# Kernel optimization log

Hardware: AMD Instinct MI355X
Metric: run time of the kernel (lower is better)

Reference implementation:

```python
import jax, jax.numpy as jnp
import numpy as np

K = 3            # CRF kernel size
THETA0 = 0.5     # color bandwidth
THETA1 = 30.0    # spatial bandwidth
ALPHA0 = 3.0     # kernel scale
BASE = 0.45      # label clamping base
CRF_ITERS = 10   # mean-field iterations
NMS_SIGMA = 2.0  # gaussian matrix-NMS sigma


def _unfold(x, k=K):
    # torch.nn.Unfold(k, stride=1, padding=k//2): (B, C, H, W) -> (B, C, k*k, H*W)
    B, C, H, W = x.shape
    p = k // 2
    xp = jnp.pad(x, ((0, 0), (0, 0), (p, p), (p, p)))
    patches = jnp.stack([xp[:, :, i:i + H, j:j + W]
                         for i in range(k) for j in range(k)], axis=2)
    return patches.reshape(B, C, k * k, H * W)


def _matrix_nms(seg_masks, cate_labels, cate_scores, sigma=NMS_SIGMA):
    n = seg_masks.shape[0]
    m = seg_masks.reshape(n, -1).astype(jnp.float32)
    sum_m = m.sum(axis=1)                         # (n,)
    inter = m @ m.T                               # (n, n)
    union = sum_m[None, :] + sum_m[:, None] - inter
    triu = jnp.triu(jnp.ones((n, n), dtype=bool), k=1)
    iou = jnp.where(triu, inter / union, 0.0)
    label_eq = (cate_labels[None, :] == cate_labels[:, None]) & triu
    decay_iou = jnp.where(label_eq, iou, 0.0)
    comp = decay_iou.max(axis=0)                  # compensate IoU per candidate
    decay = jnp.exp(-sigma * decay_iou ** 2)
    compm = jnp.exp(-sigma * comp ** 2)[:, None]  # broadcast over columns (torch expand+T)
    coef = (decay / compm).min(axis=0)
    return cate_scores * coef


def _crf(feature_map, x, targets):
    B, C, H, W = feature_map.shape
    k2 = K * K
    # gaussian pairwise kernel from (shifted) color features
    fm = feature_map + 10.0
    uf = _unfold(fm)                              # (B, C, k2, H*W)
    idx = np.arange(k2)
    spatial = ((idx // K - K // 2) ** 2 + (idx % K - K // 2) ** 2).astype(np.float32)
    color = -((uf - fm.reshape(B, C, 1, H * W)) ** 2).sum(axis=1) / (2.0 * THETA0 ** 2)
    kernel = ALPHA0 * jnp.exp(color - jnp.asarray(spatial)[None, :, None] / (2.0 * THETA1 ** 2))
    kernel = kernel[:, None]                      # (B, 1, k2, H*W)

    # unary init
    xt = x * targets
    xt = (xt > 0.5).astype(jnp.float32) * (1.0 - 2.0 * BASE) + BASE
    ret = jnp.concatenate([1.0 - xt, xt], axis=1)  # (B, 2, H, W)
    ones_t = jnp.ones_like(targets)
    for _ in range(CRF_ITERS):
        uf_x = _unfold(-jnp.log(ret.reshape(2 * B, 1, H, W))).reshape(B, 2, k2, H * W)
        aggre = (uf_x * kernel).sum(axis=2)        # (B, 2, H*W)
        f = jnp.exp(-aggre).reshape(B, 2, H, W)
        f = f * jnp.concatenate([ones_t, targets], axis=1)  # gate fg channel by targets
        f = f + 1e-6
        f = f / f.sum(axis=1, keepdims=True)
        ret = (f > 0.5).astype(jnp.float32) * (1.0 - 2.0 * BASE) + BASE
    masks = (ret[:, 1:] > 0.5).astype(jnp.float32)  # (B, 1, H, W)
    count = masks.reshape(B, -1).sum(axis=1)
    valid = ((count >= H * W * 0.05) & (count <= H * W * 0.95)).astype(jnp.float32)
    return masks, valid


def setup_inputs() -> dict:
    key = jax.random.key(0)
    k1, k2, k3, k4, k5, k6 = jax.random.split(key, 6)
    n, h, w = 256, 128, 128
    ni, c = 64, 3
    seg_masks = (jax.random.uniform(k1, (n, h, w)) > 0.5).astype(jnp.float32)
    cate_scores = jnp.sort(jax.random.uniform(k2, (n,)))[::-1]
    feature_map = jax.random.uniform(k3, (ni, c, h, w))
    x = jax.random.uniform(k4, (ni, 1, h, w))
    targets = (jax.random.uniform(k5, (ni, 1, h, w)) > 0.3).astype(jnp.float32)
    cate_labels = jax.random.randint(k6, (n,), 0, 80, dtype=jnp.int64)
    return {"seg_masks": seg_masks, "cate_scores": cate_scores,
            "feature_map": feature_map, "x": x, "targets": targets,
            "cate_labels": cate_labels}


def reference(seg_masks, cate_scores, feature_map, x, targets, cate_labels):
    scores = _matrix_nms(seg_masks, cate_labels, cate_scores)
    masks, valid = _crf(feature_map, x, targets)
    return scores, masks, valid
```

## Files before the change

kernel.cpp:

```cpp
#include <hip/hip_runtime.h>
#include <stdint.h>

#define HW 16384
#define NI 64
#define NM 256
#define WORDS 256

#define PR 136
#define WROWS 52
#define PSZ (WROWS * PR)
#define SR 34

#define LDS_PLANE_BYTES (4 * PSZ * 4)
#define LDS_STW_BYTES   (2 * WROWS * SR * 4)
#define LDS_TOTAL       (LDS_PLANE_BYTES + LDS_STW_BYTES + 64)

#define OFF_PACKED (2u << 20)
#define OFF_DIOUT  0x280000u
#define OFF_COMPM  0x2C0000u
#define OFF_CNT    0x2C1000u

__device__ __forceinline__ void build_planes_row(
    const float* __restrict__ fb, float* __restrict__ plane, const int y,
    const int xc, const int wrow, const int q, const bool inimg) {
    #pragma clang fp contract(off)
    float c0[4], c1[4], c2[4];
    if (inimg) {
        const int pp = y * 128 + xc;
        float4 cv0 = *(const float4*)&fb[pp];
        float4 cv1 = *(const float4*)&fb[HW + pp];
        float4 cv2 = *(const float4*)&fb[2 * HW + pp];
        c0[0]=cv0.x+10.0f; c0[1]=cv0.y+10.0f; c0[2]=cv0.z+10.0f; c0[3]=cv0.w+10.0f;
        c1[0]=cv1.x+10.0f; c1[1]=cv1.y+10.0f; c1[2]=cv1.z+10.0f; c1[3]=cv1.w+10.0f;
        c2[0]=cv2.x+10.0f; c2[1]=cv2.y+10.0f; c2[2]=cv2.z+10.0f; c2[3]=cv2.w+10.0f;
    }
    #pragma unroll
    for (int k = 0; k < 4; ++k) {
        const int dy = (k < 3) ? -1 : 0;
        const int dx = (k < 3) ? (k - 1) : -1;
        float res[4] = {0.0f, 0.0f, 0.0f, 0.0f};
        if (inimg) {
            const int ny = y + dy;
            if ((unsigned)ny < 128u) {
                #pragma unroll
                for (int j = 0; j < 4; ++j) {
                    const int nx = xc + j + dx;
                    if ((unsigned)nx < 128u) {
                        const int qq = ny * 128 + nx;
                        float u0 = fb[qq] + 10.0f;
                        float u1 = fb[HW + qq] + 10.0f;
                        float u2 = fb[2 * HW + qq] + 10.0f;
                        float d0 = u0 - c0[j], d1 = u1 - c1[j], d2 = u2 - c2[j];
                        float ss = d0 * d0;
                        ss = ss + d1 * d1;
                        ss = ss + d2 * d2;
                        float color = (-ss) / 0.5f;
                        float sp = (float)(dy * dy + dx * dx) / 1800.0f;
                        res[j] = 3.0f * expf(color - sp);
                    }
                }
            }
        }
        *(float4*)&plane[k * PSZ + wrow * PR + 4 + xc] =
            make_float4(res[0], res[1], res[2], res[3]);
        if (q == 0)
            *(float4*)&plane[k * PSZ + wrow * PR + 0] = make_float4(0, 0, 0, 0);
        if (q == 31)
            *(float4*)&plane[k * PSZ + wrow * PR + 132] = make_float4(0, 0, 0, 0);
    }
}

__device__ __forceinline__ void stage_init_row(
    const float* __restrict__ x, const float* __restrict__ targets,
    uint32_t* __restrict__ stw0, uint32_t* __restrict__ stw1, const int img,
    const int y, const int wrow, const int q, const int xc, const bool inimg) {
    #pragma clang fp contract(off)
    uint32_t st = 0;
    if (inimg) {
        const size_t gp = (size_t)img * HW + y * 128 + xc;
        const float4 xv = *(const float4*)(x + gp);
        const float4 tv = *(const float4*)(targets + gp);
        float xs[4] = {xv.x, xv.y, xv.z, xv.w};
        float ts[4] = {tv.x, tv.y, tv.z, tv.w};
        #pragma unroll
        for (int j = 0; j < 4; ++j) {
            float xt = xs[j] * ts[j];
            int b1 = (xt > 0.5f) ? 1 : 0;
            int tb = (ts[j] > 0.5f) ? 1 : 0;
            st |= (uint32_t)(b1 | ((b1 ^ 1) << 1) | (tb << 2)) << (8 * j);
        }
    }
    stw0[wrow * SR + 1 + q] = st;
    if (!inimg) stw1[wrow * SR + 1 + q] = 0;
    if (q == 0)  { stw0[wrow * SR + 0]  = 0; stw1[wrow * SR + 0]  = 0; }
    if (q == 31) { stw0[wrow * SR + 33] = 0; stw1[wrow * SR + 33] = 0; }
}

__device__ __forceinline__ uint32_t crf_core(const float (&kw)[9][4],
                                             const uint32_t (&in9)[9]) {
    #pragma clang fp contract(off)
    const float l45 = 0.7985076962177716f;
    const float l55 = 0.5978370007556204f;
    const uint32_t wcen = in9[4];
    float lx1r[3][6], lx0r[3][6];
    #pragma unroll
    for (int r = 0; r < 3; ++r) {
        const uint32_t wm = in9[r * 3 + 0];
        const uint32_t wc = in9[r * 3 + 1];
        const uint32_t wp = in9[r * 3 + 2];
        unsigned char b[6];
        b[0] = wm >> 24;
        b[1] = wc & 0xff; b[2] = (wc >> 8) & 0xff;
        b[3] = (wc >> 16) & 0xff; b[4] = wc >> 24;
        b[5] = wp & 0xff;
        #pragma unroll
        for (int m = 0; m < 6; ++m) {
            lx1r[r][m] = (b[m] & 1) ? l55 : l45;
            lx0r[r][m] = (b[m] & 2) ? l55 : l45;
        }
    }
    float a0[4] = {0.f, 0.f, 0.f, 0.f}, a1[4] = {0.f, 0.f, 0.f, 0.f};
    #pragma unroll
    for (int k = 0; k < 9; ++k) {
        const int r = k / 3, m0 = k % 3;
        #pragma unroll
        for (int j = 0; j < 4; ++j) {
            const float kwv = kw[k][j];
            const float t1 = lx1r[r][j + m0] * kwv;
            const float t0 = lx0r[r][j + m0] * kwv;
            a1[j] = a1[j] + t1;
            a0[j] = a0[j] + t0;
        }
    }
    uint32_t ow = 0;
    #pragma unroll
    for (int j = 0; j < 4; ++j) {
        const unsigned char sc = (wcen >> (8 * j)) & 0xffu;
        const float tval = (sc & 4) ? 1.0f : 0.0f;
        const float e1 = expf(-a1[j]);
        const float e0 = expf(-a0[j]);
        const float m1 = e1 * tval;
        const float f1 = m1 + 1e-6f;
        const float f0 = e0 + 1e-6f;
        const float den = f0 + f1;
        const float r1 = f1 / den;
        const float r0v = f0 / den;
        const int s1 = (r1 > 0.5f) ? 1 : 0;
        const int s0 = (r0v > 0.5f) ? 1 : 0;
        ow |= (uint32_t)(s1 | (s0 << 1) | (sc & 4)) << (8 * j);
    }
    return ow;
}

__global__ __launch_bounds__(832, 4) void crf10_kernel(
    const float* __restrict__ feat, const float* __restrict__ seg,
    unsigned long long* __restrict__ packed, const float* __restrict__ x,
    const float* __restrict__ targets, float* __restrict__ out,
    int* __restrict__ counters) {
    #pragma clang fp contract(off)
    extern __shared__ char smem[];
    float* plane = (float*)smem;
    uint32_t* stw0 = (uint32_t*)(smem + LDS_PLANE_BYTES);
    uint32_t* stw1 = stw0 + WROWS * SR;
    int* chg = (int*)(smem + LDS_PLANE_BYTES + LDS_STW_BYTES);
    uint32_t* const stwb[2] = {stw0, stw1};

    const int tid = threadIdx.x, bid = blockIdx.x;
    const int img = bid >> 2;
    const int r0 = (bid & 3) * 32;
    const int relp = tid >> 5;
    const int q = tid & 31;
    const int xc = q * 4;
    const int wrowA = 2 * relp, wrowB = 2 * relp + 1;
    const int yA = r0 - 10 + wrowA, yB = yA + 1;
    const bool inA = (unsigned)yA < 128u, inB = (unsigned)yB < 128u;
    const int rbaseA = wrowA * PR + 4 + xc, rbaseB = wrowB * PR + 4 + xc;
    const int sbaseA = wrowA * SR + 1 + q,  sbaseB = wrowB * SR + 1 + q;
    const float* fb = feat + (size_t)img * 3 * HW;

    {
        const int wave = tid >> 6, lane = tid & 63;
        const int gw = bid * 13 + wave;
        for (int gwi = gw; gwi < 65536; gwi += 3328) {
            const int i = gwi >> 8, w = gwi & 255;
            float v = seg[(size_t)i * HW + w * 64 + lane];
            unsigned long long m = __ballot(v > 0.5f);
            if (lane == 0) packed[w * NM + i] = m;
        }
    }

    build_planes_row(fb, plane, yA, xc, wrowA, q, inA);
    build_planes_row(fb, plane, yB, xc, wrowB, q, inB);
    stage_init_row(x, targets, stw0, stw1, img, yA, wrowA, q, xc, inA);
    stage_init_row(x, targets, stw0, stw1, img, yB, wrowB, q, xc, inB);
    if (tid < 10) chg[tid] = 0;
    __syncthreads();

    const float4 a_p0 = *(const float4*)&plane[0 * PSZ + rbaseA];
    const float4 a_p1 = *(const float4*)&plane[1 * PSZ + rbaseA];
    const float4 a_p2 = *(const float4*)&plane[2 * PSZ + rbaseA];
    const float4 a_p3 = *(const float4*)&plane[3 * PSZ + rbaseA];
    const float  a_s5 = plane[3 * PSZ + rbaseA + 4];
    const float4 b_p0 = *(const float4*)&plane[0 * PSZ + rbaseB];
    const float4 b_p1 = *(const float4*)&plane[1 * PSZ + rbaseB];
    const float4 b_p2 = *(const float4*)&plane[2 * PSZ + rbaseB];
    const float4 b_p3 = *(const float4*)&plane[3 * PSZ + rbaseB];
    const float  b_s5 = plane[3 * PSZ + rbaseB + 4];
    const float  b_s6 = plane[2 * PSZ + rbaseB - 1];
    const float  b_s8 = plane[0 * PSZ + rbaseB + 4];
    const float kwA[9][4] = {
        {a_p0.x, a_p0.y, a_p0.z, a_p0.w},
        {a_p1.x, a_p1.y, a_p1.z, a_p1.w},
        {a_p2.x, a_p2.y, a_p2.z, a_p2.w},
        {a_p3.x, a_p3.y, a_p3.z, a_p3.w},
        {3.0f, 3.0f, 3.0f, 3.0f},
        {a_p3.y, a_p3.z, a_p3.w, a_s5},
        {b_s6, b_p2.x, b_p2.y, b_p2.z},
        {b_p1.x, b_p1.y, b_p1.z, b_p1.w},
        {b_p0.y, b_p0.z, b_p0.w, b_s8}};

    uint32_t pinA[9], pinB[9];
    uint32_t powvA = 0, powvB = 0;
    bool hpA = false, hpB = false;
    int cur = 0;
    for (int s = 0; s < 10; ++s) {
        const int lo = (r0 - 9 + s < 0) ? 0 : r0 - 9 + s;
        const int hi = (r0 + 41 - s > 128) ? 128 : r0 + 41 - s;
        const bool actA = (yA >= lo) && (yA < hi);
        const bool actB = (yB >= lo) && (yB < hi);
        const uint32_t* sw = stwb[cur];
        uint32_t* swn = stwb[cur ^ 1];
        bool changed = false;
        if (actA || actB) {
            const uint32_t ra0 = sw[sbaseA - 1], ra1 = sw[sbaseA], ra2 = sw[sbaseA + 1];
            const uint32_t rb0 = sw[sbaseB - 1], rb1 = sw[sbaseB], rb2 = sw[sbaseB + 1];
            if (actA) {
                const uint32_t in9[9] = {sw[sbaseA - SR - 1], sw[sbaseA - SR],
                                         sw[sbaseA - SR + 1], ra0, ra1, ra2,
                                         rb0, rb1, rb2};
                bool same = hpA;
                #pragma unroll
                for (int m = 0; m < 9; ++m) same = same && (in9[m] == pinA[m]);
                uint32_t ow;
                if (same) {
                    ow = powvA;
                } else {
                    ow = crf_core(kwA, in9);
                    #pragma unroll
                    for (int m = 0; m < 9; ++m) pinA[m] = in9[m];
                    powvA = ow;
                    hpA = true;
                }
                swn[sbaseA] = ow;
                changed = (ow != ra1);
            }
            if (actB) {
                const uint32_t in9[9] = {ra0, ra1, ra2, rb0, rb1, rb2,
                                         sw[sbaseB + SR - 1], sw[sbaseB + SR],
                                         sw[sbaseB + SR + 1]};
                bool same = hpB;
                #pragma unroll
                for (int m = 0; m < 9; ++m) same = same && (in9[m] == pinB[m]);
                uint32_t ow;
                if (same) {
                    ow = powvB;
                } else {
                    const float4 c_p0 = *(const float4*)&plane[0 * PSZ + rbaseB + PR];
                    const float4 c_p1 = *(const float4*)&plane[1 * PSZ + rbaseB + PR];
                    const float4 c_p2 = *(const float4*)&plane[2 * PSZ + rbaseB + PR];
                    const float  c_s6 = plane[2 * PSZ + rbaseB + PR - 1];
                    const float  c_s8 = plane[0 * PSZ + rbaseB + PR + 4];
                    const float kwB[9][4] = {
                        {b_p0.x, b_p0.y, b_p0.z, b_p0.w},
                        {b_p1.x, b_p1.y, b_p1.z, b_p1.w},
                        {b_p2.x, b_p2.y, b_p2.z, b_p2.w},
                        {b_p3.x, b_p3.y, b_p3.z, b_p3.w},
                        {3.0f, 3.0f, 3.0f, 3.0f},
                        {b_p3.y, b_p3.z, b_p3.w, b_s5},
                        {c_s6, c_p2.x, c_p2.y, c_p2.z},
                        {c_p1.x, c_p1.y, c_p1.z, c_p1.w},
                        {c_p0.y, c_p0.z, c_p0.w, c_s8}};
                    ow = crf_core(kwB, in9);
                    #pragma unroll
                    for (int m = 0; m < 9; ++m) pinB[m] = in9[m];
                    powvB = ow;
                    hpB = true;
                }
                swn[sbaseB] = ow;
                changed = changed || (ow != rb1);
            }
        }
        unsigned long long bal = __ballot(changed);
        if ((tid & 63) == 0 && bal) atomicOr(&chg[s], 1);
        __syncthreads();
        if (chg[s] == 0) break;
        cur ^= 1;
    }

    int cnt = 0;
    {
        const uint32_t* swf = stwb[cur];
        float* om = out + NM + (size_t)img * HW;
        if (yA >= r0 && yA < r0 + 32) {
            const uint32_t w = swf[sbaseA];
            *(float4*)(om + yA * 128 + xc) =
                make_float4((float)(w & 1), (float)((w >> 8) & 1),
                            (float)((w >> 16) & 1), (float)((w >> 24) & 1));
            cnt += __popc(w & 0x01010101u);
        }
        if (yB >= r0 && yB < r0 + 32) {
            const uint32_t w = swf[sbaseB];
            *(float4*)(om + yB * 128 + xc) =
                make_float4((float)(w & 1), (float)((w >> 8) & 1),
                            (float)((w >> 16) & 1), (float)((w >> 24) & 1));
            cnt += __popc(w & 0x01010101u);
        }
    }
    __syncthreads();
    {
        int* cred = (int*)plane;
        cred[tid] = cnt;
        if (tid < 192) cred[832 + tid] = 0;
        __syncthreads();
        for (int off = 512; off > 0; off >>= 1) {
            if (tid < off) cred[tid] += cred[tid + off];
            __syncthreads();
        }
        if (tid == 0) counters[bid] = cred[0];
    }
}

__global__ __launch_bounds__(256) void diou_compm_kernel(
    const unsigned long long* __restrict__ packed, const int* __restrict__ labels,
    float* __restrict__ diouT, float* __restrict__ compm) {
    #pragma clang fp contract(off)
    __shared__ unsigned long long colj[WORDS];
    __shared__ float red[NM];
    const int j = blockIdx.x, i = threadIdx.x;
    colj[i] = packed[i * NM + j];
    __syncthreads();
    int inter = 0, si = 0, sj = 0;
    for (int w = 0; w < WORDS; ++w) {
        unsigned long long a = colj[w];
        unsigned long long b = packed[w * NM + i];
        inter += __popcll(a & b);
        sj += __popcll(a);
        si += __popcll(b);
    }
    float d = 0.0f;
    if (j > i && labels[i] == labels[j]) {
        float u = (float)(si + sj - inter);
        d = (float)inter / u;
    }
    diouT[j * NM + i] = d;
    red[i] = d;
    __syncthreads();
    for (int off = 128; off > 0; off >>= 1) {
        if (i < off) red[i] = fmaxf(red[i], red[i + off]);
        __syncthreads();
    }
    if (i == 0) {
        float m = red[0];
        float t = m * m;
        compm[j] = expf(-2.0f * t);
    }
}

__global__ __launch_bounds__(256) void coef_valid_kernel(
    const float* __restrict__ scores, const float* __restrict__ diouT,
    const float* __restrict__ compm, const int* __restrict__ counters,
    float* __restrict__ out) {
    #pragma clang fp contract(off)
    __shared__ float red[NM];
    const int bid = blockIdx.x, tid = threadIdx.x;
    float d = diouT[bid * NM + tid];
    float dd = d * d;
    float dec = expf(-2.0f * dd);
    red[tid] = dec / compm[tid];
    __syncthreads();
    for (int off = 128; off > 0; off >>= 1) {
        if (tid < off) red[tid] = fminf(red[tid], red[tid + off]);
        __syncthreads();
    }
    if (tid == 0) out[bid] = scores[bid] * red[0];
    if (bid == 0 && tid < NI) {
        int c = counters[4 * tid] + counters[4 * tid + 1] +
                counters[4 * tid + 2] + counters[4 * tid + 3];
        out[NM + (size_t)NI * HW + tid] = (c >= 820 && c <= 15564) ? 1.0f : 0.0f;
    }
}

extern "C" void kernel_launch(void* const* d_in, const int* in_sizes, int n_in,
                              void* d_out, int out_size, void* d_ws, size_t ws_size,
                              hipStream_t stream) {
    const float* seg = (const float*)d_in[0];
    const float* cate_scores = (const float*)d_in[1];
    const float* feat = (const float*)d_in[2];
    const float* x = (const float*)d_in[3];
    const float* targets = (const float*)d_in[4];
    const int* labels = (const int*)d_in[5];
    float* out = (float*)d_out;
    char* ws = (char*)d_ws;

    unsigned long long* packed = (unsigned long long*)(ws + OFF_PACKED);
    float* diouT = (float*)(ws + OFF_DIOUT);
    float* compm = (float*)(ws + OFF_COMPM);
    int* counters = (int*)(ws + OFF_CNT);

    static bool attr_done = false;
    if (!attr_done) {
        (void)hipFuncSetAttribute((const void*)crf10_kernel,
                                  hipFuncAttributeMaxDynamicSharedMemorySize,
                                  LDS_TOTAL);
        attr_done = true;
    }

    crf10_kernel<<<256, 832, LDS_TOTAL, stream>>>(feat, seg, packed, x, targets,
                                                  out, counters);
    diou_compm_kernel<<<NM, 256, 0, stream>>>(packed, labels, diouT, compm);
    coef_valid_kernel<<<NM, 256, 0, stream>>>(cate_scores, diouT, compm,
                                              counters, out);
}
```

Measured before the change: 167.3 us.

## Split CRF tiles into 16-row blocks and keep kernel weights in registers

The CRF kernel now processes 16 output rows per block instead of 32, using 512 blocks of 576 threads, and shrinks the halo window to 36 rows. Pairwise weight planes are kept in registers, and neighbour values are fetched with warp shuffles. Only three planes for the next row are staged in a smaller static LDS strip, replacing the large dynamic LDS plane buffer. This is meant to cut LDS use, raise occupancy and use more CUs, but it adds halo recomputation overhead: 20 halo rows per 16 output rows instead of per 32.

```diff
diff --git a/kernel.cpp b/kernel.cpp
--- a/kernel.cpp
+++ b/kernel.cpp
@@ -7,22 +7,22 @@
 #define WORDS 256
 
 #define PR 136
-#define WROWS 52
-#define PSZ (WROWS * PR)
+#define TROWS 16
+#define WROWS 36
+#define NTHREADS 576
+#define NBLK 512
 #define SR 34
-
-#define LDS_PLANE_BYTES (4 * PSZ * 4)
-#define LDS_STW_BYTES   (2 * WROWS * SR * 4)
-#define LDS_TOTAL       (LDS_PLANE_BYTES + LDS_STW_BYTES + 64)
+#define SPR 19
+#define SPSZ (SPR * PR)
 
 #define OFF_PACKED (2u << 20)
 #define OFF_DIOUT  0x280000u
 #define OFF_COMPM  0x2C0000u
 #define OFF_CNT    0x2C1000u
 
-__device__ __forceinline__ void build_planes_row(
-    const float* __restrict__ fb, float* __restrict__ plane, const int y,
-    const int xc, const int wrow, const int q, const bool inimg) {
+__device__ __forceinline__ void build_row(
+    const float* __restrict__ fb, const int y, const int xc, const bool inimg,
+    float4 (&out)[4]) {
     #pragma clang fp contract(off)
     float c0[4], c1[4], c2[4];
     if (inimg) {
@@ -61,12 +61,7 @@
                 }
             }
         }
-        *(float4*)&plane[k * PSZ + wrow * PR + 4 + xc] =
-            make_float4(res[0], res[1], res[2], res[3]);
-        if (q == 0)
-            *(float4*)&plane[k * PSZ + wrow * PR + 0] = make_float4(0, 0, 0, 0);
-        if (q == 31)
-            *(float4*)&plane[k * PSZ + wrow * PR + 132] = make_float4(0, 0, 0, 0);
+        out[k] = make_float4(res[0], res[1], res[2], res[3]);
     }
 }
 
@@ -152,36 +147,33 @@
     return ow;
 }
 
-__global__ __launch_bounds__(832, 4) void crf10_kernel(
+__global__ __launch_bounds__(576, 4) void crf10_kernel(
     const float* __restrict__ feat, const float* __restrict__ seg,
     unsigned long long* __restrict__ packed, const float* __restrict__ x,
     const float* __restrict__ targets, float* __restrict__ out,
     int* __restrict__ counters) {
     #pragma clang fp contract(off)
-    extern __shared__ char smem[];
-    float* plane = (float*)smem;
-    uint32_t* stw0 = (uint32_t*)(smem + LDS_PLANE_BYTES);
-    uint32_t* stw1 = stw0 + WROWS * SR;
-    int* chg = (int*)(smem + LDS_PLANE_BYTES + LDS_STW_BYTES);
-    uint32_t* const stwb[2] = {stw0, stw1};
+    __shared__ float strip[3 * SPSZ];
+    __shared__ uint32_t stw0[WROWS * SR];
+    __shared__ uint32_t stw1[WROWS * SR];
+    __shared__ int chg[10];
 
     const int tid = threadIdx.x, bid = blockIdx.x;
-    const int img = bid >> 2;
-    const int r0 = (bid & 3) * 32;
+    const int img = bid >> 3;
+    const int r0 = (bid & 7) * TROWS;
     const int relp = tid >> 5;
     const int q = tid & 31;
     const int xc = q * 4;
-    const int wrowA = 2 * relp, wrowB = 2 * relp + 1;
+    const int wrowA = 2 * relp, wrowB = wrowA + 1;
     const int yA = r0 - 10 + wrowA, yB = yA + 1;
     const bool inA = (unsigned)yA < 128u, inB = (unsigned)yB < 128u;
-    const int rbaseA = wrowA * PR + 4 + xc, rbaseB = wrowB * PR + 4 + xc;
-    const int sbaseA = wrowA * SR + 1 + q,  sbaseB = wrowB * SR + 1 + q;
+    const int sbaseA = wrowA * SR + 1 + q, sbaseB = wrowB * SR + 1 + q;
     const float* fb = feat + (size_t)img * 3 * HW;
 
     {
         const int wave = tid >> 6, lane = tid & 63;
-        const int gw = bid * 13 + wave;
-        for (int gwi = gw; gwi < 65536; gwi += 3328) {
+        const int gw = bid * 9 + wave;
+        for (int gwi = gw; gwi < 65536; gwi += 4608) {
             const int i = gwi >> 8, w = gwi & 255;
             float v = seg[(size_t)i * HW + w * 64 + lane];
             unsigned long long m = __ballot(v > 0.5f);
@@ -189,35 +181,37 @@
         }
     }
 
-    build_planes_row(fb, plane, yA, xc, wrowA, q, inA);
-    build_planes_row(fb, plane, yB, xc, wrowB, q, inB);
+    float4 ap[4], bp[4];
+    build_row(fb, yA, xc, inA, ap);
+    build_row(fb, yB, xc, inB, bp);
+    #pragma unroll
+    for (int k = 0; k < 3; ++k) {
+        *(float4*)&strip[k * SPSZ + relp * PR + 4 + xc] = ap[k];
+        if (q == 0)
+            *(float4*)&strip[k * SPSZ + relp * PR + 0] = make_float4(0, 0, 0, 0);
+        if (q == 31)
+            *(float4*)&strip[k * SPSZ + relp * PR + 132] = make_float4(0, 0, 0, 0);
+    }
     stage_init_row(x, targets, stw0, stw1, img, yA, wrowA, q, xc, inA);
     stage_init_row(x, targets, stw0, stw1, img, yB, wrowB, q, xc, inB);
     if (tid < 10) chg[tid] = 0;
+
+    float a_s5 = __shfl_down(ap[3].x, 1); if (q == 31) a_s5 = 0.0f;
+    float b_s5 = __shfl_down(bp[3].x, 1); if (q == 31) b_s5 = 0.0f;
+    float b_s6 = __shfl_up(bp[2].w, 1);   if (q == 0)  b_s6 = 0.0f;
+    float b_s8 = __shfl_down(bp[0].x, 1); if (q == 31) b_s8 = 0.0f;
     __syncthreads();
 
-    const float4 a_p0 = *(const float4*)&plane[0 * PSZ + rbaseA];
-    const float4 a_p1 = *(const float4*)&plane[1 * PSZ + rbaseA];
-    const float4 a_p2 = *(const float4*)&plane[2 * PSZ + rbaseA];
-    const float4 a_p3 = *(const float4*)&plane[3 * PSZ + rbaseA];
-    const float  a_s5 = plane[3 * PSZ + rbaseA + 4];
-    const float4 b_p0 = *(const float4*)&plane[0 * PSZ + rbaseB];
-    const float4 b_p1 = *(const float4*)&plane[1 * PSZ + rbaseB];
-    const float4 b_p2 = *(const float4*)&plane[2 * PSZ + rbaseB];
-    const float4 b_p3 = *(const float4*)&plane[3 * PSZ + rbaseB];
-    const float  b_s5 = plane[3 * PSZ + rbaseB + 4];
-    const float  b_s6 = plane[2 * PSZ + rbaseB - 1];
-    const float  b_s8 = plane[0 * PSZ + rbaseB + 4];
     const float kwA[9][4] = {
-        {a_p0.x, a_p0.y, a_p0.z, a_p0.w},
-        {a_p1.x, a_p1.y, a_p1.z, a_p1.w},
-        {a_p2.x, a_p2.y, a_p2.z, a_p2.w},
-        {a_p3.x, a_p3.y, a_p3.z, a_p3.w},
+        {ap[0].x, ap[0].y, ap[0].z, ap[0].w},
+        {ap[1].x, ap[1].y, ap[1].z, ap[1].w},
+        {ap[2].x, ap[2].y, ap[2].z, ap[2].w},
+        {ap[3].x, ap[3].y, ap[3].z, ap[3].w},
         {3.0f, 3.0f, 3.0f, 3.0f},
-        {a_p3.y, a_p3.z, a_p3.w, a_s5},
-        {b_s6, b_p2.x, b_p2.y, b_p2.z},
-        {b_p1.x, b_p1.y, b_p1.z, b_p1.w},
-        {b_p0.y, b_p0.z, b_p0.w, b_s8}};
+        {ap[3].y, ap[3].z, ap[3].w, a_s5},
+        {b_s6, bp[2].x, bp[2].y, bp[2].z},
+        {bp[1].x, bp[1].y, bp[1].z, bp[1].w},
+        {bp[0].y, bp[0].z, bp[0].w, b_s8}};
 
     uint32_t pinA[9], pinB[9];
     uint32_t powvA = 0, powvB = 0;
@@ -225,11 +219,11 @@
     int cur = 0;
     for (int s = 0; s < 10; ++s) {
         const int lo = (r0 - 9 + s < 0) ? 0 : r0 - 9 + s;
-        const int hi = (r0 + 41 - s > 128) ? 128 : r0 + 41 - s;
+        const int hi = (r0 + 25 - s > 128) ? 128 : r0 + 25 - s;
         const bool actA = (yA >= lo) && (yA < hi);
         const bool actB = (yB >= lo) && (yB < hi);
-        const uint32_t* sw = stwb[cur];
-        uint32_t* swn = stwb[cur ^ 1];
+        const uint32_t* sw = cur ? stw1 : stw0;
+        uint32_t* swn = cur ? stw0 : stw1;
         bool changed = false;
         if (actA || actB) {
             const uint32_t ra0 = sw[sbaseA - 1], ra1 = sw[sbaseA], ra2 = sw[sbaseA + 1];
@@ -265,18 +259,19 @@
                 if (same) {
                     ow = powvB;
                 } else {
-                    const float4 c_p0 = *(const float4*)&plane[0 * PSZ + rbaseB + PR];
-                    const float4 c_p1 = *(const float4*)&plane[1 * PSZ + rbaseB + PR];
-                    const float4 c_p2 = *(const float4*)&plane[2 * PSZ + rbaseB + PR];
-                    const float  c_s6 = plane[2 * PSZ + rbaseB + PR - 1];
-                    const float  c_s8 = plane[0 * PSZ + rbaseB + PR + 4];
+                    const int cb = (relp + 1) * PR + 4 + xc;
+                    const float4 c_p0 = *(const float4*)&strip[0 * SPSZ + cb];
+                    const float4 c_p1 = *(const float4*)&strip[1 * SPSZ + cb];
+                    const float4 c_p2 = *(const float4*)&strip[2 * SPSZ + cb];
+                    const float  c_s6 = strip[2 * SPSZ + cb - 1];
+                    const float  c_s8 = strip[0 * SPSZ + cb + 4];
                     const float kwB[9][4] = {
-                        {b_p0.x, b_p0.y, b_p0.z, b_p0.w},
-                        {b_p1.x, b_p1.y, b_p1.z, b_p1.w},
-                        {b_p2.x, b_p2.y, b_p2.z, b_p2.w},
-                        {b_p3.x, b_p3.y, b_p3.z, b_p3.w},
+                        {bp[0].x, bp[0].y, bp[0].z, bp[0].w},
+                        {bp[1].x, bp[1].y, bp[1].z, bp[1].w},
+                        {bp[2].x, bp[2].y, bp[2].z, bp[2].w},
+                        {bp[3].x, bp[3].y, bp[3].z, bp[3].w},
                         {3.0f, 3.0f, 3.0f, 3.0f},
-                        {b_p3.y, b_p3.z, b_p3.w, b_s5},
+                        {bp[3].y, bp[3].z, bp[3].w, b_s5},
                         {c_s6, c_p2.x, c_p2.y, c_p2.z},
                         {c_p1.x, c_p1.y, c_p1.z, c_p1.w},
                         {c_p0.y, c_p0.z, c_p0.w, c_s8}};
@@ -299,16 +294,16 @@
 
     int cnt = 0;
     {
-        const uint32_t* swf = stwb[cur];
+        const uint32_t* swf = cur ? stw1 : stw0;
         float* om = out + NM + (size_t)img * HW;
-        if (yA >= r0 && yA < r0 + 32) {
+        if (yA >= r0 && yA < r0 + TROWS) {
             const uint32_t w = swf[sbaseA];
             *(float4*)(om + yA * 128 + xc) =
                 make_float4((float)(w & 1), (float)((w >> 8) & 1),
                             (float)((w >> 16) & 1), (float)((w >> 24) & 1));
             cnt += __popc(w & 0x01010101u);
         }
-        if (yB >= r0 && yB < r0 + 32) {
+        if (yB >= r0 && yB < r0 + TROWS) {
             const uint32_t w = swf[sbaseB];
             *(float4*)(om + yB * 128 + xc) =
                 make_float4((float)(w & 1), (float)((w >> 8) & 1),
@@ -318,9 +313,9 @@
     }
     __syncthreads();
     {
-        int* cred = (int*)plane;
+        int* cred = (int*)strip;
         cred[tid] = cnt;
-        if (tid < 192) cred[832 + tid] = 0;
+        if (tid < 448) cred[576 + tid] = 0;
         __syncthreads();
         for (int off = 512; off > 0; off >>= 1) {
             if (tid < off) cred[tid] += cred[tid + off];
@@ -384,8 +379,9 @@
     }
     if (tid == 0) out[bid] = scores[bid] * red[0];
     if (bid == 0 && tid < NI) {
-        int c = counters[4 * tid] + counters[4 * tid + 1] +
-                counters[4 * tid + 2] + counters[4 * tid + 3];
+        int c = 0;
+        #pragma unroll
+        for (int t = 0; t < 8; ++t) c += counters[8 * tid + t];
         out[NM + (size_t)NI * HW + tid] = (c >= 820 && c <= 15564) ? 1.0f : 0.0f;
     }
 }
@@ -407,16 +403,8 @@
     float* compm = (float*)(ws + OFF_COMPM);
     int* counters = (int*)(ws + OFF_CNT);
 
-    static bool attr_done = false;
-    if (!attr_done) {
-        (void)hipFuncSetAttribute((const void*)crf10_kernel,
-                                  hipFuncAttributeMaxDynamicSharedMemorySize,
-                                  LDS_TOTAL);
-        attr_done = true;
-    }
-
-    crf10_kernel<<<256, 832, LDS_TOTAL, stream>>>(feat, seg, packed, x, targets,
-                                                  out, counters);
+    crf10_kernel<<<NBLK, NTHREADS, 0, stream>>>(feat, seg, packed, x, targets,
+                                                out, counters);
     diou_compm_kernel<<<NM, 256, 0, stream>>>(packed, labels, diouT, compm);
     coef_valid_kernel<<<NM, 256, 0, stream>>>(cate_scores, diouT, compm,
                                               counters, out);
```

Result: slower. 206.5 us (+23.4%).
